# Optimization experiments

Measured on AMD Instinct MI355X. Metric: run time of the kernel, lower is better.

The kernel has to match this reference:

```python
import jax, jax.numpy as jnp
import numpy as np

N, D, H, K = 4096, 256, 4, 16

def setup_inputs() -> dict:
    key = jax.random.key(0)
    ks = jax.random.split(key, 6)
    return {
        "query":     jax.random.normal(ks[0], (N, D), dtype=jnp.float32),
        "key_value": jax.random.normal(ks[1], (N, D), dtype=jnp.float32),
        "W_q": jax.random.normal(ks[2], (H, D, K), dtype=jnp.float32) * 0.05,
        "W_k": jax.random.normal(ks[3], (H, D, K), dtype=jnp.float32) * 0.05,
        "W_v": jax.random.normal(ks[4], (H, D, K), dtype=jnp.float32) * 0.05,
        "W_o": jax.random.normal(ks[5], (H * K, D), dtype=jnp.float32) * 0.05,
    }

def reference(query, key_value, W_q, W_k, W_v, W_o):
    # Per-head projections, batched over heads: [H, N, K]
    Q = jnp.einsum('nd,hdk->hnk', query, W_q)
    Kh = jnp.einsum('nd,hdk->hnk', key_value, W_k)
    V = jnp.einsum('nd,hdk->hnk', key_value, W_v)
    scale = jnp.sqrt(jnp.asarray(K, dtype=Q.dtype))
    scores = jnp.einsum('hnk,hmk->hnm', Q, Kh) / scale  # [H, N, N]
    attn = jax.nn.softmax(scores, axis=-1)
    heads = jnp.einsum('hnm,hmk->hnk', attn, V)         # [H, N, K]
    # concat heads along last dim (head-major order) -> [N, H*K]
    concat = jnp.transpose(heads, (1, 0, 2)).reshape(query.shape[0], -1)
    return concat @ W_o  # [N, D]
```

## Files before the change

kernel.cpp:

```cpp
#include <hip/hip_runtime.h>
#include <hip/hip_bf16.h>

#define NN 4096
#define DD 256
#define HH 4
#define KK 16
#define SPLIT 8

typedef short bf16x4 __attribute__((ext_vector_type(4)));
typedef float f32x4 __attribute__((ext_vector_type(4)));

__device__ __forceinline__ unsigned short bf16c(float f) {
  __hip_bfloat16 h = __float2bfloat16(f);
  return *reinterpret_cast<unsigned short*>(&h);
}

__device__ __forceinline__ float fexp2(float x) {
#if __has_builtin(__builtin_amdgcn_exp2f)
  return __builtin_amdgcn_exp2f(x);
#else
  return exp2f(x);
#endif
}

__device__ __forceinline__ f32x4 mfma16_bf16(bf16x4 a, bf16x4 b, f32x4 c) {
#if __has_builtin(__builtin_amdgcn_mfma_f32_16x16x16bf16_1k)
  return __builtin_amdgcn_mfma_f32_16x16x16bf16_1k(a, b, c, 0, 0, 0);
#else
  f32x4 d;
  asm volatile("v_mfma_f32_16x16x16_bf16 %0, %1, %2, %3\n\ts_nop 7\n\ts_nop 7"
               : "=&v"(d) : "v"(a), "v"(b), "v"(c));
  return d;
#endif
}

__global__ __launch_bounds__(64) void wfrag_kernel(
    const float* __restrict__ Wq, const float* __restrict__ Wk,
    const float* __restrict__ Wv, unsigned short* __restrict__ wf) {
  const int b = blockIdx.x;
  const int mat = b >> 6, h = (b >> 4) & 3, kstep = b & 15;
  const int l = threadIdx.x;
  const int lx = l & 15, g = l >> 4;
  const float* W = (mat == 0) ? Wq : (mat == 1 ? Wk : Wv);
  const float scale = (mat == 0) ? 0.25f * 1.4426950408889634f : 1.0f;
  unsigned short* dst = wf + ((size_t)b * 64 + l) * 4;
  #pragma unroll
  for (int j = 0; j < 4; j++) {
    int d = kstep * 16 + g * 4 + j;
    dst[j] = bf16c(W[(size_t)h * DD * KK + (size_t)d * KK + lx] * scale);
  }
}

__global__ __launch_bounds__(256) void proj_gemm_kernel(
    const float* __restrict__ query, const float* __restrict__ kvin,
    const unsigned short* __restrict__ wf,
    unsigned short* __restrict__ Qb, unsigned short* __restrict__ Kb,
    unsigned short* __restrict__ Vt) {
  const int tid = threadIdx.x;
  const int w = tid >> 6, l = tid & 63;
  const int lx = l & 15, g = l >> 4;
  const int id = blockIdx.x * 4 + w;
  const int qt = id / 12, ns = id % 12;
  const int mat = ns >> 2, h = ns & 3;
  const float* src = (mat == 0) ? query : kvin;
  const unsigned short* wfb = wf + (size_t)((mat * 4 + h) * 16) * 64 * 4;
  const float* arow = src + (size_t)(qt * 16 + lx) * DD + g * 4;

  f32x4 acc = {0.f, 0.f, 0.f, 0.f};
  #pragma unroll
  for (int ks = 0; ks < 16; ks++) {
    float4 a0 = *(const float4*)(arow + ks * 16);
    bf16x4 af;
    af[0] = (short)bf16c(a0.x); af[1] = (short)bf16c(a0.y);
    af[2] = (short)bf16c(a0.z); af[3] = (short)bf16c(a0.w);
    bf16x4 bfr = *(const bf16x4*)(wfb + ((size_t)ks * 64 + l) * 4);
    acc = mfma16_bf16(af, bfr, acc);
  }
  if (mat < 2) {
    unsigned short* dstp = (mat == 0) ? Qb : Kb;
    #pragma unroll
    for (int r = 0; r < 4; r++) {
      int n = qt * 16 + g * 4 + r;
      dstp[((size_t)h * NN + n) * KK + lx] = bf16c(acc[r]);
    }
  } else {
    #pragma unroll
    for (int r = 0; r < 4; r++) {
      int n = qt * 16 + g * 4 + r;
      Vt[((size_t)h * KK + lx) * NN + n] = bf16c(acc[r]);
    }
  }
}

__global__ __launch_bounds__(256) void attn_kernel(
    const unsigned short* __restrict__ Qb, const unsigned short* __restrict__ Kb,
    const unsigned short* __restrict__ Vt, float* __restrict__ pbuf) {
  const int tid = threadIdx.x;
  const int w = tid >> 6, l = tid & 63;
  const int lx = l & 15, g = l >> 4;
  const int h = blockIdx.y, sp = blockIdx.z;
  const int kb0 = sp * (NN / SPLIT);
  const int q0 = blockIdx.x * 128 + w * 32;

  bf16x4 qfa = *(const bf16x4*)(Qb + ((size_t)h * NN + q0 + lx) * KK + g * 4);
  bf16x4 qfb = *(const bf16x4*)(Qb + ((size_t)h * NN + q0 + 16 + lx) * KK + g * 4);

  const unsigned short* kptr = Kb + ((size_t)h * NN + kb0 + lx) * KK + g * 4;
  const unsigned short* vptr = Vt + ((size_t)h * KK + lx) * NN + kb0 + g * 4;
  f32x4 c2a = {0.f, 0.f, 0.f, 0.f}, c2b = {0.f, 0.f, 0.f, 0.f};
  const f32x4 zero4 = {0.f, 0.f, 0.f, 0.f};
  float ssa = 0.f, ssb = 0.f;

  #pragma unroll 4
  for (int tile = 0; tile < NN / SPLIT / 16; tile++) {
    bf16x4 kf = *(const bf16x4*)kptr;
    kptr += 16 * KK;
    bf16x4 vf = *(const bf16x4*)vptr;
    vptr += 16;

    f32x4 c1a = mfma16_bf16(kf, qfa, zero4);
    f32x4 c1b = mfma16_bf16(kf, qfb, zero4);
    bf16x4 pa, pb;
    #pragma unroll
    for (int r = 0; r < 4; r++) {
      float ea = fexp2(c1a[r]);
      float eb = fexp2(c1b[r]);
      ssa += ea; ssb += eb;
      pa[r] = (short)bf16c(ea);
      pb[r] = (short)bf16c(eb);
    }
    c2a = mfma16_bf16(vf, pa, c2a);
    c2b = mfma16_bf16(vf, pb, c2b);
  }

  ssa += __shfl_xor(ssa, 16); ssa += __shfl_xor(ssa, 32);
  ssb += __shfl_xor(ssb, 16); ssb += __shfl_xor(ssb, 32);

  size_t ba = ((size_t)(h * NN + q0 + lx) * SPLIT + sp) * 17;
  size_t bb = ((size_t)(h * NN + q0 + 16 + lx) * SPLIT + sp) * 17;
  #pragma unroll
  for (int r = 0; r < 4; r++) {
    pbuf[ba + g * 4 + r] = c2a[r];
    pbuf[bb + g * 4 + r] = c2b[r];
  }
  if (g == 0) { pbuf[ba + 16] = ssa; pbuf[bb + 16] = ssb; }
}

__global__ __launch_bounds__(256) void reduce_out_kernel(
    const float* __restrict__ pbuf, const float* __restrict__ Wo,
    float* __restrict__ out) {
  __shared__ float cc[8][64];
  const int tid = threadIdx.x;
  const int n0  = blockIdx.x * 8;

  for (int it = tid; it < 512; it += 256) {
    int r = it >> 6;
    int j = it & 63;
    int h = j >> 4;
    int kk2 = j & 15;
    size_t hn = (size_t)h * NN + n0 + r;
    float num = 0.f, den = 0.f;
    #pragma unroll
    for (int s2 = 0; s2 < SPLIT; s2++) {
      const float* p = pbuf + (hn * SPLIT + s2) * 17;
      num += p[kk2];
      den += p[16];
    }
    cc[r][j] = num / den;
  }
  __syncthreads();

  float acc[8];
  #pragma unroll
  for (int r = 0; r < 8; r++) acc[r] = 0.f;
  for (int j = 0; j < 64; j++) {
    float wv = Wo[(size_t)j * DD + tid];
    #pragma unroll
    for (int r = 0; r < 8; r++) acc[r] = fmaf(cc[r][j], wv, acc[r]);
  }
  #pragma unroll
  for (int r = 0; r < 8; r++)
    out[(size_t)(n0 + r) * DD + tid] = acc[r];
}

extern "C" void kernel_launch(void* const* d_in, const int* in_sizes, int n_in,
                              void* d_out, int out_size, void* d_ws, size_t ws_size,
                              hipStream_t stream) {
  const float* query = (const float*)d_in[0];
  const float* kv    = (const float*)d_in[1];
  const float* Wq    = (const float*)d_in[2];
  const float* Wk    = (const float*)d_in[3];
  const float* Wv    = (const float*)d_in[4];
  const float* Wo    = (const float*)d_in[5];
  float* out = (float*)d_out;

  unsigned short* Qb = (unsigned short*)d_ws;
  unsigned short* Kb = Qb + (size_t)HH * NN * KK;
  unsigned short* Vt = Kb + (size_t)HH * NN * KK;
  unsigned short* wf = Vt + (size_t)HH * NN * KK;
  float* pbuf = (float*)((char*)d_ws +
                         2u * (3u * HH * NN * KK + 192u * 64u * 4u));

  hipLaunchKernelGGL(wfrag_kernel, dim3(192), dim3(64), 0, stream, Wq, Wk, Wv, wf);
  hipLaunchKernelGGL(proj_gemm_kernel, dim3(768), dim3(256), 0, stream,
                     query, kv, wf, Qb, Kb, Vt);
  hipLaunchKernelGGL(attn_kernel, dim3(NN / 128, HH, SPLIT), dim3(256), 0, stream,
                     Qb, Kb, Vt, pbuf);
  hipLaunchKernelGGL(reduce_out_kernel, dim3(NN / 8), dim3(256), 0, stream,
                     pbuf, Wo, out);
}
```

Before: 109.0 us.

## Fuse weight fragment prep into projection, tile V layout, compute rowsum via MFMA

Removes the separate weight-fragment kernel by having each projection block build its bf16 weight fragments in shared memory, which saves one launch but repeats that conversion in every block. V is now stored in 16-key tiles so each lane reads contiguous bf16x4 chunks in the attention loop instead of strided rows. The softmax denominator is accumulated with an extra MFMA against a ones vector rather than scalar adds and cross-lane shuffles. This trades VALU work for MFMA work in the inner loop.

```diff
diff --git a/kernel.cpp b/kernel.cpp
--- a/kernel.cpp
+++ b/kernel.cpp
@@ -34,36 +34,34 @@
 #endif
 }
 
-__global__ __launch_bounds__(64) void wfrag_kernel(
-    const float* __restrict__ Wq, const float* __restrict__ Wk,
-    const float* __restrict__ Wv, unsigned short* __restrict__ wf) {
-  const int b = blockIdx.x;
-  const int mat = b >> 6, h = (b >> 4) & 3, kstep = b & 15;
-  const int l = threadIdx.x;
-  const int lx = l & 15, g = l >> 4;
-  const float* W = (mat == 0) ? Wq : (mat == 1 ? Wk : Wv);
-  const float scale = (mat == 0) ? 0.25f * 1.4426950408889634f : 1.0f;
-  unsigned short* dst = wf + ((size_t)b * 64 + l) * 4;
-  #pragma unroll
-  for (int j = 0; j < 4; j++) {
-    int d = kstep * 16 + g * 4 + j;
-    dst[j] = bf16c(W[(size_t)h * DD * KK + (size_t)d * KK + lx] * scale);
-  }
-}
-
 __global__ __launch_bounds__(256) void proj_gemm_kernel(
     const float* __restrict__ query, const float* __restrict__ kvin,
-    const unsigned short* __restrict__ wf,
+    const float* __restrict__ Wq, const float* __restrict__ Wk,
+    const float* __restrict__ Wv,
     unsigned short* __restrict__ Qb, unsigned short* __restrict__ Kb,
     unsigned short* __restrict__ Vt) {
+  __shared__ unsigned short wtab[16][64][4];
   const int tid = threadIdx.x;
   const int w = tid >> 6, l = tid & 63;
   const int lx = l & 15, g = l >> 4;
-  const int id = blockIdx.x * 4 + w;
-  const int qt = id / 12, ns = id % 12;
+  const int ns = blockIdx.x >> 6;
+  const int qt = (blockIdx.x & 63) * 4 + w;
   const int mat = ns >> 2, h = ns & 3;
+  const float* W = (mat == 0) ? Wq : (mat == 1 ? Wk : Wv);
+  const float scale = (mat == 0) ? 0.25f * 1.4426950408889634f : 1.0f;
+
+  for (int slot = tid; slot < 1024; slot += 256) {
+    int ks = slot >> 6, sl = slot & 63;
+    int slx = sl & 15, sg = sl >> 4;
+    #pragma unroll
+    for (int j = 0; j < 4; j++) {
+      int d = ks * 16 + sg * 4 + j;
+      wtab[ks][sl][j] = bf16c(W[(size_t)h * DD * KK + (size_t)d * KK + slx] * scale);
+    }
+  }
+  __syncthreads();
+
   const float* src = (mat == 0) ? query : kvin;
-  const unsigned short* wfb = wf + (size_t)((mat * 4 + h) * 16) * 64 * 4;
   const float* arow = src + (size_t)(qt * 16 + lx) * DD + g * 4;
 
   f32x4 acc = {0.f, 0.f, 0.f, 0.f};
@@ -73,7 +71,7 @@
     bf16x4 af;
     af[0] = (short)bf16c(a0.x); af[1] = (short)bf16c(a0.y);
     af[2] = (short)bf16c(a0.z); af[3] = (short)bf16c(a0.w);
-    bf16x4 bfr = *(const bf16x4*)(wfb + ((size_t)ks * 64 + l) * 4);
+    bf16x4 bfr = *(const bf16x4*)&wtab[ks][l][0];
     acc = mfma16_bf16(af, bfr, acc);
   }
   if (mat < 2) {
@@ -84,11 +82,10 @@
       dstp[((size_t)h * NN + n) * KK + lx] = bf16c(acc[r]);
     }
   } else {
-    #pragma unroll
-    for (int r = 0; r < 4; r++) {
-      int n = qt * 16 + g * 4 + r;
-      Vt[((size_t)h * KK + lx) * NN + n] = bf16c(acc[r]);
-    }
+    bf16x4 vv;
+    #pragma unroll
+    for (int r = 0; r < 4; r++) vv[r] = (short)bf16c(acc[r]);
+    *(bf16x4*)(Vt + (((size_t)h * (NN / 16) + qt) * 16 + lx) * 16 + g * 4) = vv;
   }
 }
 
@@ -106,35 +103,34 @@
   bf16x4 qfb = *(const bf16x4*)(Qb + ((size_t)h * NN + q0 + 16 + lx) * KK + g * 4);
 
   const unsigned short* kptr = Kb + ((size_t)h * NN + kb0 + lx) * KK + g * 4;
-  const unsigned short* vptr = Vt + ((size_t)h * KK + lx) * NN + kb0 + g * 4;
+  const unsigned short* vptr =
+      Vt + (((size_t)h * (NN / 16) + (kb0 >> 4)) * 16 + lx) * 16 + g * 4;
   f32x4 c2a = {0.f, 0.f, 0.f, 0.f}, c2b = {0.f, 0.f, 0.f, 0.f};
+  f32x4 csa = {0.f, 0.f, 0.f, 0.f}, csb = {0.f, 0.f, 0.f, 0.f};
   const f32x4 zero4 = {0.f, 0.f, 0.f, 0.f};
-  float ssa = 0.f, ssb = 0.f;
+  const short one_bf = (short)0x3F80;
+  const bf16x4 onesf = {one_bf, one_bf, one_bf, one_bf};
 
   #pragma unroll 4
   for (int tile = 0; tile < NN / SPLIT / 16; tile++) {
     bf16x4 kf = *(const bf16x4*)kptr;
     kptr += 16 * KK;
     bf16x4 vf = *(const bf16x4*)vptr;
-    vptr += 16;
+    vptr += 256;
 
     f32x4 c1a = mfma16_bf16(kf, qfa, zero4);
     f32x4 c1b = mfma16_bf16(kf, qfb, zero4);
     bf16x4 pa, pb;
     #pragma unroll
     for (int r = 0; r < 4; r++) {
-      float ea = fexp2(c1a[r]);
-      float eb = fexp2(c1b[r]);
-      ssa += ea; ssb += eb;
-      pa[r] = (short)bf16c(ea);
-      pb[r] = (short)bf16c(eb);
+      pa[r] = (short)bf16c(fexp2(c1a[r]));
+      pb[r] = (short)bf16c(fexp2(c1b[r]));
     }
     c2a = mfma16_bf16(vf, pa, c2a);
     c2b = mfma16_bf16(vf, pb, c2b);
-  }
-
-  ssa += __shfl_xor(ssa, 16); ssa += __shfl_xor(ssa, 32);
-  ssb += __shfl_xor(ssb, 16); ssb += __shfl_xor(ssb, 32);
+    csa = mfma16_bf16(onesf, pa, csa);
+    csb = mfma16_bf16(onesf, pb, csb);
+  }
 
   size_t ba = ((size_t)(h * NN + q0 + lx) * SPLIT + sp) * 17;
   size_t bb = ((size_t)(h * NN + q0 + 16 + lx) * SPLIT + sp) * 17;
@@ -143,7 +139,7 @@
     pbuf[ba + g * 4 + r] = c2a[r];
     pbuf[bb + g * 4 + r] = c2b[r];
   }
-  if (g == 0) { pbuf[ba + 16] = ssa; pbuf[bb + 16] = ssb; }
+  if (g == 0) { pbuf[ba + 16] = csa[0]; pbuf[bb + 16] = csb[0]; }
 }
 
 __global__ __launch_bounds__(256) void reduce_out_kernel(
@@ -197,13 +193,10 @@
   unsigned short* Qb = (unsigned short*)d_ws;
   unsigned short* Kb = Qb + (size_t)HH * NN * KK;
   unsigned short* Vt = Kb + (size_t)HH * NN * KK;
-  unsigned short* wf = Vt + (size_t)HH * NN * KK;
-  float* pbuf = (float*)((char*)d_ws +
-                         2u * (3u * HH * NN * KK + 192u * 64u * 4u));
-
-  hipLaunchKernelGGL(wfrag_kernel, dim3(192), dim3(64), 0, stream, Wq, Wk, Wv, wf);
+  float* pbuf = (float*)((char*)d_ws + 2u * (3u * HH * NN * KK));
+
   hipLaunchKernelGGL(proj_gemm_kernel, dim3(768), dim3(256), 0, stream,
-                     query, kv, wf, Qb, Kb, Vt);
+                     query, kv, Wq, Wk, Wv, Qb, Kb, Vt);
   hipLaunchKernelGGL(attn_kernel, dim3(NN / 128, HH, SPLIT), dim3(256), 0, stream,
                      Qb, Kb, Vt, pbuf);
   hipLaunchKernelGGL(reduce_out_kernel, dim3(NN / 8), dim3(256), 0, stream,
```

New measurement: 97.94 us. -10.1%, faster.
